# Kernel tuning notes

Measured on AMD Instinct MI355X. Metric: run time of the kernel, lower is better.

The kernel has to match this reference:

```python
import jax, jax.numpy as jnp
import numpy as np

VOCAB = 128000; D = 128; H = 4; HD = D // H; NL = 2; DOUT = 64
MAXW = 32; B = 64; L = 64; N_ITERS = 32

def _ln(x, g, b):
    m = jnp.mean(x, -1, keepdims=True)
    v = jnp.var(x, -1, keepdims=True)
    return (x - m) * jax.lax.rsqrt(v + 1e-5) * g + b

def _encoder(x, pad, p):
    # post-norm torch TransformerEncoderLayer, relu activation. x: [N,W,D], pad True=padding key
    neg = jnp.where(pad, -1e9, 0.0)[:, None, None, :]
    n = x.shape[0]
    for l in range(NL):
        qkv = x @ p["Wqkv"][l].T + p["bqkv"][l]
        q, k, v = jnp.split(qkv, 3, axis=-1)
        q = q.reshape(n, MAXW, H, HD).transpose(0, 2, 1, 3)
        k = k.reshape(n, MAXW, H, HD).transpose(0, 2, 1, 3)
        v = v.reshape(n, MAXW, H, HD).transpose(0, 2, 1, 3)
        s = jnp.einsum('nhqd,nhkd->nhqk', q, k) * (1.0 / float(np.sqrt(HD))) + neg
        o = jnp.einsum('nhqk,nhkd->nhqd', jax.nn.softmax(s, -1), v)
        o = o.transpose(0, 2, 1, 3).reshape(n, MAXW, D) @ p["Wo"][l].T + p["bo"][l]
        x = _ln(x + o, p["ln1g"][l], p["ln1b"][l])
        f = jax.nn.relu(x @ p["W1"][l].T + p["b1"][l]) @ p["W2"][l].T + p["b2"][l]
        x = _ln(x + f, p["ln2g"][l], p["ln2b"][l])
    return x

def _forward(p, token_ids, padding_mask, key):
    seq_len = jnp.sum(~padding_mask, 1).astype(jnp.int32)
    pos_idx = jnp.arange(MAXW)
    bidx = jnp.arange(B)

    def _head(x, W1h, b1h, W2h, b2h):
        return (jax.nn.relu(x @ W1h.T + b1h) @ W2h.T + b2h)[:, 0]

    def _gru(x, h):
        gi = x @ p["gru_Wih"].T + p["gru_bih"]
        gh = h @ p["gru_Whh"].T + p["gru_bhh"]
        ir, iz, inn = jnp.split(gi, 3, -1)
        hr, hz, hn = jnp.split(gh, 3, -1)
        r = jax.nn.sigmoid(ir + hr)
        z = jax.nn.sigmoid(iz + hz)
        return (1.0 - z) * jnp.tanh(inn + r * hn) + z * h

    def step(carry, k):
        win_ids, win_len, input_pos, gru_h, done = carry
        active = ~done
        pad = ~((pos_idx[None, :] < win_len[:, None]) & active[:, None])
        pad = pad.at[:, 0].set(False)  # keep softmax finite for empty windows; t1 zeroed below
        x = p["tok_emb"][win_ids] + p["pos_emb"][None, :, :]
        enc = _encoder(x, pad, p)
        last = enc[bidx, jnp.maximum(win_len - 1, 0)]
        vec = last @ p["proj_W"].T + p["proj_b"]
        vec = vec / jnp.maximum(jnp.linalg.norm(vec, axis=-1, keepdims=True), 1e-12)
        nonempty = (win_len > 0) & active
        t1 = jnp.where(nonempty[:, None], vec, 0.0)
        gru_h = jnp.where(active[:, None], _gru(t1, gru_h), gru_h)
        has_input = active & (input_pos < seq_len)
        nt = token_ids[bidx, jnp.clip(input_pos, 0, L - 1)]
        next_embs = jnp.where(has_input[:, None], p["tok_emb"][nt], 0.0)
        acc_l = _head(jnp.concatenate([next_embs, t1, gru_h], 1), p["acc_W1"], p["acc_b1"], p["acc_W2"], p["acc_b2"])
        tg = jnp.concatenate([t1, gru_h], 1)
        emt_l = _head(tg, p["emt_W1"], p["emt_b1"], p["emt_W2"], p["emt_b2"])
        evt_l = _head(tg, p["evt_W1"], p["evt_b1"], p["evt_W2"], p["evt_b2"])
        k1, k2, k3 = jax.random.split(k, 3)
        acc_s = jax.random.bernoulli(k1, jax.nn.sigmoid(acc_l))
        emt_s = jax.random.bernoulli(k2, jax.nn.sigmoid(emt_l))
        evt_s = jax.random.bernoulli(k3, jax.nn.sigmoid(evt_l))
        lp = jnp.stack([jax.nn.log_sigmoid(jnp.where(acc_s, acc_l, -acc_l)),
                        jax.nn.log_sigmoid(jnp.where(emt_s, emt_l, -emt_l)),
                        jax.nn.log_sigmoid(jnp.where(evt_s, evt_l, -evt_l))], 1)
        dec = jnp.stack([acc_s, emt_s, evt_s], 1).astype(jnp.float32)
        a = acc_s & has_input
        e = emt_s & nonempty
        v = evt_s & nonempty
        none = active & ~(a | e | v)
        a = a | (none & has_input)
        e = e | (none & ~has_input & (win_len > 0))
        a_eff = a & (win_len < MAXW)
        win_ids = jnp.where(a_eff[:, None] & (pos_idx[None, :] == win_len[:, None]), nt[:, None], win_ids)
        input_pos = input_pos + a_eff.astype(jnp.int32)
        win_len = win_len + a_eff.astype(jnp.int32)
        emit_event = e & (win_len > 0)
        v_eff = v & (win_len > 0)
        win_ids = jnp.where(v_eff[:, None], jnp.roll(win_ids, -1, axis=1), win_ids)
        win_len = win_len - v_eff.astype(jnp.int32)
        done = done | (active & (input_pos >= seq_len) & (win_len == 0))
        return (win_ids, win_len, input_pos, gru_h, done), (t1, lp, dec, emit_event)

    init = (jnp.zeros((B, MAXW), dtype=token_ids.dtype), jnp.zeros(B, jnp.int32), jnp.zeros(B, jnp.int32),
            jnp.zeros((B, D), jnp.float32), seq_len == 0)
    keys = jax.random.split(key, N_ITERS)
    _, (t1s, lps, decs, emits) = jax.lax.scan(step, init, keys)
    return t1s, lps, decs, jnp.sum(emits.astype(jnp.int32), 0)

def setup_inputs():
    key = jax.random.key(0)
    ks = jax.random.split(key, 20)
    def rn(k, shape):
        return jax.random.normal(k, shape, jnp.float32) * 0.02
    inp = {}
    inp["token_ids"] = jax.random.randint(ks[0], (B, L), 0, VOCAB)
    inp["padding_mask"] = jnp.zeros((B, L), dtype=bool)
    inp["token_instr_idx"] = jax.random.randint(ks[1], (B, L), 0, 32)
    inp["n_instructions"] = jax.random.randint(ks[2], (B,), 1, 32)
    inp["tok_emb"] = rn(ks[3], (VOCAB, D))
    inp["pos_emb"] = rn(ks[4], (MAXW, D))
    inp["Wqkv"] = rn(ks[5], (NL, 3 * D, D)); inp["bqkv"] = jnp.zeros((NL, 3 * D))
    inp["Wo"] = rn(ks[6], (NL, D, D)); inp["bo"] = jnp.zeros((NL, D))
    inp["ln1g"] = jnp.ones((NL, D)); inp["ln1b"] = jnp.zeros((NL, D))
    inp["W1"] = rn(ks[7], (NL, 4 * D, D)); inp["b1"] = jnp.zeros((NL, 4 * D))
    inp["W2"] = rn(ks[8], (NL, D, 4 * D)); inp["b2"] = jnp.zeros((NL, D))
    inp["ln2g"] = jnp.ones((NL, D)); inp["ln2b"] = jnp.zeros((NL, D))
    inp["proj_W"] = rn(ks[9], (DOUT, D)); inp["proj_b"] = jnp.zeros((DOUT,))
    inp["gru_Wih"] = rn(ks[10], (3 * D, DOUT)); inp["gru_Whh"] = rn(ks[11], (3 * D, D))
    inp["gru_bih"] = jnp.zeros((3 * D,)); inp["gru_bhh"] = jnp.zeros((3 * D,))
    inp["acc_W1"] = rn(ks[12], (D, 2 * D + DOUT)); inp["acc_b1"] = jnp.zeros((D,))
    inp["acc_W2"] = rn(ks[13], (1, D)); inp["acc_b2"] = jnp.full((1,), 2.0)
    inp["emt_W1"] = rn(ks[14], (D, D + DOUT)); inp["emt_b1"] = jnp.zeros((D,))
    inp["emt_W2"] = rn(ks[15], (1, D)); inp["emt_b2"] = jnp.full((1,), -2.0)
    inp["evt_W1"] = rn(ks[16], (D, D + DOUT)); inp["evt_b1"] = jnp.zeros((D,))
    inp["evt_W2"] = rn(ks[17], (1, D)); inp["evt_b2"] = jnp.full((1,), -2.0)
    return inp

def reference(token_ids, padding_mask, token_instr_idx, n_instructions, tok_emb, pos_emb, Wqkv, bqkv, Wo, bo, ln1g, ln1b, W1, b1, W2, b2, ln2g, ln2b, proj_W, proj_b, gru_Wih, gru_Whh, gru_bih, gru_bhh, acc_W1, acc_b1, acc_W2, acc_b2, emt_W1, emt_b1, emt_W2, emt_b2, evt_W1, evt_b1, evt_W2, evt_b2):
    p = dict(tok_emb=tok_emb, pos_emb=pos_emb, Wqkv=Wqkv, bqkv=bqkv, Wo=Wo, bo=bo, ln1g=ln1g, ln1b=ln1b,
             W1=W1, b1=b1, W2=W2, b2=b2, ln2g=ln2g, ln2b=ln2b, proj_W=proj_W, proj_b=proj_b,
             gru_Wih=gru_Wih, gru_Whh=gru_Whh, gru_bih=gru_bih, gru_bhh=gru_bhh,
             acc_W1=acc_W1, acc_b1=acc_b1, acc_W2=acc_W2, acc_b2=acc_b2,
             emt_W1=emt_W1, emt_b1=emt_b1, emt_W2=emt_W2, emt_b2=emt_b2,
             evt_W1=evt_W1, evt_b1=evt_b1, evt_W2=evt_W2, evt_b2=evt_b2)
    # token_instr_idx / n_instructions are only used for emission bookkeeping (no tensor math); unused here.
    return _forward(p, token_ids, padding_mask, jax.random.key(42))
```

## Files before the change

kernel.cpp:

```cpp
#include <hip/hip_runtime.h>
#include <hip/hip_bf16.h>


#define XS 132
#define QS 388
#define HS 516
#define PS 36
#define NW 16

struct KParams {
  const int* token_ids;
  const unsigned char* pad;
  const void *tok_emb, *pos_emb, *Wqkv, *bqkv, *Wo, *bo, *ln1g, *ln1b;
  const void *W1, *b1, *W2, *b2, *ln2g, *ln2b, *projW, *projb;
  const void *gWih, *gWhh, *gbih, *gbhh;
  const void *accW1, *accb1, *accW2, *accb2;
  const void *emtW1, *emtb1, *emtW2, *emtb2;
  const void *evtW1, *evtb1, *evtW2, *evtb2;
  float* out;
};

struct Smem {
  float xbuf[32 * XS];
  float qh[32 * HS];
  float obuf[32 * XS];
  float pbuf[4608];
  float attT[128];
  float tva[128];
  double gild[384];
  double ghld[384];
  double hsd[128];
  double t1d[64];
  double catd[320];
  double hid2d[384];
  double logitsd[3];
  int win_ids[32];
  int sI[6];
  unsigned keyts[32][2];
};

__device__ __forceinline__ float ldw(const float* p){ return *p; }
__device__ __forceinline__ float ldw(const unsigned short* p){
  return __uint_as_float(((unsigned)*p) << 16);
}
__device__ __forceinline__ float4 ld4(const float* p){ return *(const float4*)p; }
__device__ __forceinline__ float4 ld4(const unsigned short* p){
  ushort4 u = *(const ushort4*)p;
  return make_float4(__uint_as_float((unsigned)u.x << 16),
                     __uint_as_float((unsigned)u.y << 16),
                     __uint_as_float((unsigned)u.z << 16),
                     __uint_as_float((unsigned)u.w << 16));
}
template<typename WT>
__device__ __forceinline__ double ldwd(const WT* p){ return (double)ldw(p); }

__device__ __forceinline__ float temb(const void* te, int isb, long long idx){
  if (isb) return __uint_as_float(((unsigned)((const unsigned short*)te)[idx]) << 16);
  return ((const float*)te)[idx];
}

__device__ __forceinline__ void tfry(unsigned k0, unsigned k1, unsigned x0, unsigned x1,
                                     unsigned &o0, unsigned &o1){
  unsigned ks2 = k0 ^ k1 ^ 0x1BD11BDAu;
  unsigned x = x0 + k0, y = x1 + k1;
#define TFR(r) { x += y; y = (y << r) | (y >> (32 - r)); y ^= x; }
  TFR(13) TFR(15) TFR(26) TFR(6)  x += k1;  y += ks2 + 1u;
  TFR(17) TFR(29) TFR(16) TFR(24) x += ks2; y += k0 + 2u;
  TFR(13) TFR(15) TFR(26) TFR(6)  x += k0;  y += k1 + 3u;
  TFR(17) TFR(29) TFR(16) TFR(24) x += k1;  y += ks2 + 4u;
  TFR(13) TFR(15) TFR(26) TFR(6)  x += ks2; y += k0 + 5u;
#undef TFR
  o0 = x; o1 = y;
}
__device__ __forceinline__ float u01(unsigned bits){
  return __uint_as_float((bits >> 9) | 0x3f800000u) - 1.0f;
}
__device__ __forceinline__ double logsigd(double x){
  return fmin(x, 0.0) - log1p(exp(-fabs(x)));
}
__device__ __forceinline__ float wredsum(float v, int width){
  for (int m = width >> 1; m > 0; m >>= 1) v += __shfl_xor(v, m, width);
  return v;
}
__device__ __forceinline__ double wredsumd(double v, int width){
  for (int m = width >> 1; m > 0; m >>= 1) v += __shfl_xor(v, m, width);
  return v;
}
__device__ __forceinline__ float dot4f(float4 a, float4 b){
  return a.x*b.x + a.y*b.y + a.z*b.z + a.w*b.w;
}

template<int T, int K, bool RELU, typename WT>
__device__ void gemm_tok(const WT* __restrict__ Wm, const WT* __restrict__ bias,
                         int J, const float* __restrict__ xl, int xs,
                         float* __restrict__ ol, int os, int ntok,
                         int lane, int wv, int nwv)
{
  const int JBG = J >> 6;
  const int ntt = (ntok + T - 1) / T;
  for (int item = wv; item < JBG * ntt; item += nwv) {
    const int jg = item % JBG, tt = item / JBG;
    const int j0 = jg * 64 + lane;
    float acc[T];
#pragma unroll
    for (int t = 0; t < T; ++t) acc[t] = 0.f;
    const float* xr = xl + tt * T * xs;
    const WT* wr = Wm + j0 * K;
#pragma unroll 4
    for (int k = 0; k < K; k += 4) {
      float4 w = ld4(wr + k);
      float4 xv[T];
#pragma unroll
      for (int t = 0; t < T; ++t) xv[t] = *(const float4*)(xr + t * xs + k);
#pragma unroll
      for (int t = 0; t < T; ++t)
        acc[t] += w.x * xv[t].x + w.y * xv[t].y + w.z * xv[t].z + w.w * xv[t].w;
    }
    float bj = ldw(bias + j0);
#pragma unroll
    for (int t = 0; t < T; ++t) {
      int tok = tt * T + t;
      if (tok < ntok) {
        float v = acc[t] + bj;
        if (RELU) v = fmaxf(v, 0.f);
        ol[tok * os + j0] = v;
      }
    }
  }
}

template<int K, typename WT>
__device__ __forceinline__ float dotgf(const WT* __restrict__ w, const float* x){
  float acc = 0.f;
#pragma unroll 8
  for (int k = 0; k < K; k += 4) {
    float4 wv = ld4(w + k);
    acc += wv.x * x[k] + wv.y * x[k+1] + wv.z * x[k+2] + wv.w * x[k+3];
  }
  return acc;
}
template<int K, typename WT>
__device__ __forceinline__ double dotgd(const WT* __restrict__ w, const double* x){
  double acc = 0.0;
#pragma unroll 4
  for (int k = 0; k < K; k += 4) {
    float4 wv = ld4(w + k);
    acc += (double)wv.x * x[k] + (double)wv.y * x[k+1]
         + (double)wv.z * x[k+2] + (double)wv.w * x[k+3];
  }
  return acc;
}
template<int K, typename WT>
__device__ __forceinline__ double dotgdx(const WT* __restrict__ w, const float* x){
  double acc = 0.0;
#pragma unroll 4
  for (int k = 0; k < K; k += 4) {
    float4 wv = ld4(w + k);
    acc += (double)wv.x * (double)x[k] + (double)wv.y * (double)x[k+1]
         + (double)wv.z * (double)x[k+2] + (double)wv.w * (double)x[k+3];
  }
  return acc;
}

template<typename WT>
__device__ void ln_rows(float* xb, const float* ob, const WT* __restrict__ g,
                        const WT* __restrict__ bb, int W, int tid){
  if (tid >= 256) return;
  const int i = tid >> 3, sub = tid & 7;
  const int base = i * XS + sub * 16;
  float y[16];
  float s = 0.f;
#pragma unroll
  for (int u = 0; u < 16; ++u) { y[u] = xb[base + u] + ob[base + u]; s += y[u]; }
  s = wredsum(s, 8);
  const float m = s * (1.0f / 128.0f);
  float vs = 0.f;
#pragma unroll
  for (int u = 0; u < 16; ++u) { float d = y[u] - m; vs += d * d; }
  vs = wredsum(vs, 8);
  const float rstd = 1.0f / sqrtf(vs * (1.0f / 128.0f) + 1e-5f);
  if (i < W) {
#pragma unroll
    for (int u = 0; u < 16; ++u)
      xb[base + u] = (y[u] - m) * rstd * ldw(g + sub * 16 + u) + ldw(bb + sub * 16 + u);
  }
}
template<typename WT>
__device__ __forceinline__ void ln_tail(float* xrow, const float* add,
                                        const WT* __restrict__ g,
                                        const WT* __restrict__ bb, int tid){
  if (tid < 64) {
    float y0 = xrow[tid] + add[tid];
    float y1 = xrow[64 + tid] + add[64 + tid];
    float m = wredsum(y0 + y1, 64) * (1.0f / 128.0f);
    float d0 = y0 - m, d1 = y1 - m;
    float rstd = 1.0f / sqrtf(wredsum(d0 * d0 + d1 * d1, 64) * (1.0f / 128.0f) + 1e-5f);
    xrow[tid] = d0 * rstd * ldw(g + tid) + ldw(bb + tid);
    xrow[64 + tid] = d1 * rstd * ldw(g + 64 + tid) + ldw(bb + 64 + tid);
  }
}

template<typename WT>
__device__ void run_all(const KParams& P, Smem& S, int row, int tid, int isbEmb){
  const WT* pos_emb = (const WT*)P.pos_emb;
  const WT* Wqkv = (const WT*)P.Wqkv;   const WT* bqkv = (const WT*)P.bqkv;
  const WT* Wo = (const WT*)P.Wo;       const WT* bo = (const WT*)P.bo;
  const WT* ln1g = (const WT*)P.ln1g;   const WT* ln1b = (const WT*)P.ln1b;
  const WT* W1 = (const WT*)P.W1;       const WT* b1 = (const WT*)P.b1;
  const WT* W2 = (const WT*)P.W2;       const WT* b2 = (const WT*)P.b2;
  const WT* ln2g = (const WT*)P.ln2g;   const WT* ln2b = (const WT*)P.ln2b;
  const WT* projW = (const WT*)P.projW; const WT* projb = (const WT*)P.projb;
  const WT* gWih = (const WT*)P.gWih;   const WT* gWhh = (const WT*)P.gWhh;
  const WT* gbih = (const WT*)P.gbih;   const WT* gbhh = (const WT*)P.gbhh;
  const WT* accW1 = (const WT*)P.accW1; const WT* accb1 = (const WT*)P.accb1;
  const WT* accW2 = (const WT*)P.accW2; const WT* accb2 = (const WT*)P.accb2;
  const WT* emtW1 = (const WT*)P.emtW1; const WT* emtb1 = (const WT*)P.emtb1;
  const WT* emtW2 = (const WT*)P.emtW2; const WT* emtb2 = (const WT*)P.emtb2;
  const WT* evtW1 = (const WT*)P.evtW1; const WT* evtb1 = (const WT*)P.evtb1;
  const WT* evtW2 = (const WT*)P.evtW2; const WT* evtb2 = (const WT*)P.evtb2;

  const int lane = tid & 63, wid = tid >> 6;

  if (tid == 0) {
    int seq = 0;
    for (int l = 0; l < 64; ++l) seq += (P.pad[row * 64 + l] == 0);
    S.sI[0] = 0; S.sI[1] = 0; S.sI[2] = (seq == 0) ? 1 : 0; S.sI[3] = seq; S.sI[4] = 0;
  }
  if (tid < 128) S.hsd[tid] = 0.0;
  if (tid < 32) {
    S.win_ids[tid] = 0;
    unsigned a0, a1;
    tfry(0u, 42u, 0u, (unsigned)tid, a0, a1);
    S.keyts[tid][0] = a0; S.keyts[tid][1] = a1;
  }
  __syncthreads();

  for (int t = 0; t < 32; ++t) {
    const int wl = S.sI[0], ip = S.sI[1], done = S.sI[2], seq = S.sI[3];
    const int act = !done;
    const int W = wl;
    const int enc = (act && wl > 0) ? 1 : 0;
    const int jl = (W > 0) ? (W - 1) : 0;

    if (enc) {
      for (int idx = tid; idx < W * 128; idx += 1024) {
        int i = idx >> 7, d = idx & 127;
        S.xbuf[i * XS + d] = temb(P.tok_emb, isbEmb, (long long)S.win_ids[i] * 128 + d)
                             + ldw(pos_emb + i * 128 + d);
      }
      __syncthreads();
      gemm_tok<8, 128, false>(Wqkv, bqkv, 384, S.xbuf, XS, S.qh, QS, W, lane, wid, NW);
      __syncthreads();
      if (tid < 128) {
        int h = tid >> 5, i = tid & 31;
        if (i < W) {
          float4 q[8];
#pragma unroll
          for (int kk = 0; kk < 8; ++kk) q[kk] = *(const float4*)&S.qh[i * QS + h * 32 + kk * 4];
          int pb = (h * 32 + i) * PS;
          float m = -1e30f;
          for (int j = 0; j < W; ++j) {
            float s = 0.f;
#pragma unroll
            for (int kk = 0; kk < 8; ++kk)
              s += dot4f(q[kk], *(const float4*)&S.qh[j * QS + 128 + h * 32 + kk * 4]);
            s *= 0.17677669529663687f;
            S.pbuf[pb + j] = s;
            m = fmaxf(m, s);
          }
          float sum = 0.f;
          for (int j = 0; j < W; ++j) { float e = expf(S.pbuf[pb + j] - m); S.pbuf[pb + j] = e; sum += e; }
          float rs = 1.0f / sum;
          for (int j = 0; j < W; ++j) S.pbuf[pb + j] *= rs;
        }
      }
      __syncthreads();
      {
        int c = tid & 127, qsub = tid >> 7, h = c >> 5;
        for (int i = qsub; i < W; i += 8) {
          float acc = 0.f;
          for (int j = 0; j < W; ++j) acc += S.pbuf[(h * 32 + i) * PS + j] * S.qh[j * QS + 256 + c];
          S.obuf[i * XS + c] = acc;
        }
      }
      __syncthreads();
      gemm_tok<4, 128, false>(Wo, bo, 128, S.obuf, XS, S.pbuf, XS, W, lane, wid, NW);
      __syncthreads();
      ln_rows(S.xbuf, S.pbuf, ln1g, ln1b, W, tid);
      __syncthreads();
      gemm_tok<8, 128, true>(W1, b1, 512, S.xbuf, XS, S.qh, HS, W, lane, wid, NW);
      __syncthreads();
      gemm_tok<8, 512, false>(W2, b2, 128, S.qh, HS, S.obuf, XS, W, lane, wid, NW);
      __syncthreads();
      ln_rows(S.xbuf, S.obuf, ln2g, ln2b, W, tid);
      __syncthreads();
      {
        const WT* Wq = Wqkv + 384 * 128;
        const WT* bq = bqkv + 384;
        if (wid < 14) {
          gemm_tok<8, 128, false>(Wq + 128 * 128, bq + 128, 256,
                                  S.xbuf, XS, S.qh + 128, QS, W, lane, wid, 14);
        } else {
          int j = tid - 896;
          S.qh[jl * QS + j] = ldw(bq + j) + dotgf<128>(Wq + j * 128, &S.xbuf[jl * XS]);
        }
        __syncthreads();
        if (tid < 128) {
          int h = tid >> 5, j = tid & 31;
          float s = -1e30f;
          if (j < W) {
            s = 0.f;
#pragma unroll
            for (int kk = 0; kk < 8; ++kk)
              s += dot4f(*(const float4*)&S.qh[jl * QS + h * 32 + kk * 4],
                         *(const float4*)&S.qh[j * QS + 128 + h * 32 + kk * 4]);
            s *= 0.17677669529663687f;
          }
          float m = s;
          for (int mk = 16; mk; mk >>= 1) m = fmaxf(m, __shfl_xor(m, mk, 32));
          float e = (j < W) ? expf(s - m) : 0.f;
          float sum = e;
          for (int mk = 16; mk; mk >>= 1) sum += __shfl_xor(sum, mk, 32);
          if (j < W) S.pbuf[h * PS + j] = e * (1.0f / sum);
        }
        __syncthreads();
        if (tid < 128) {
          int h = tid >> 5;
          float acc = 0.f;
          for (int j = 0; j < W; ++j) acc += S.pbuf[h * PS + j] * S.qh[j * QS + 256 + tid];
          S.attT[tid] = acc;
        }
        __syncthreads();
        if (tid < 128)
          S.tva[tid] = ldw(bo + 128 + tid) + dotgf<128>(Wo + 16384 + tid * 128, S.attT);
        __syncthreads();
        ln_tail(&S.xbuf[jl * XS], S.tva, ln1g + 128, ln1b + 128, tid);
        __syncthreads();
        if (tid < 512)
          S.qh[tid] = fmaxf(ldw(b1 + 512 + tid) + dotgf<128>(W1 + (512 + tid) * 128, &S.xbuf[jl * XS]), 0.f);
        __syncthreads();
        if (tid < 128)
          S.tva[tid] = ldw(b2 + 128 + tid) + dotgf<512>(W2 + (128 + tid) * 512, S.qh);
        __syncthreads();
        ln_tail(&S.xbuf[jl * XS], S.tva, ln2g + 128, ln2b + 128, tid);
        __syncthreads();
      }
    }

    if (tid < 64) {
      double tv = 0.0;
      if (enc) {
        double v = ldwd(projb + tid) + dotgdx<128>(projW + tid * 128, &S.xbuf[jl * XS]);
        double ss = wredsumd(v * v, 64);
        tv = v / fmax(sqrt(ss), 1e-12);
      }
      S.t1d[tid] = tv;
      S.catd[128 + tid] = tv;
      P.out[(size_t)t * 4096 + row * 64 + tid] = (float)tv;
    } else if (tid >= 384 && tid < 768) {
      if (act) {
        int j = tid - 384;
        S.ghld[j] = ldwd(gbhh + j) + dotgd<128>(gWhh + j * 128, S.hsd);
      }
    } else if (tid >= 768 && tid < 896) {
      int j = tid - 768;
      int ipc = ip < 0 ? 0 : (ip > 63 ? 63 : ip);
      int nt = P.token_ids[row * 64 + ipc];
      int has_in = (act && (ip < seq)) ? 1 : 0;
      S.catd[j] = has_in ? (double)temb(P.tok_emb, isbEmb, (long long)nt * 128 + j) : 0.0;
    }
    __syncthreads();

    if (act) {
      if (tid < 384)
        S.gild[tid] = ldwd(gbih + tid) + dotgd<64>(gWih + tid * 64, S.t1d);
      __syncthreads();
    }

    if (tid < 128) {
      if (act) {
        double r = 1.0 / (1.0 + exp(-(S.gild[tid] + S.ghld[tid])));
        double z = 1.0 / (1.0 + exp(-(S.gild[128 + tid] + S.ghld[128 + tid])));
        double n = tanh(S.gild[256 + tid] + r * S.ghld[256 + tid]);
        S.hsd[tid] = (1.0 - z) * n + z * S.hsd[tid];
      }
      S.catd[192 + tid] = S.hsd[tid];
    }
    __syncthreads();

    if (tid < 128) {
      S.hid2d[tid] = fmax(ldwd(accb1 + tid) + dotgd<320>(accW1 + tid * 320, S.catd), 0.0);
    } else if (tid < 256) {
      int j = tid - 128;
      S.hid2d[128 + j] = fmax(ldwd(emtb1 + j) + dotgd<192>(emtW1 + j * 192, S.catd + 128), 0.0);
    } else if (tid < 384) {
      int j = tid - 256;
      S.hid2d[256 + j] = fmax(ldwd(evtb1 + j) + dotgd<192>(evtW1 + j * 192, S.catd + 128), 0.0);
    }
    __syncthreads();

    {
      int hw = tid >> 6;
      if (hw < 3) {
        int ln = tid & 63;
        const WT* w2 = (hw == 0) ? accW2 : ((hw == 1) ? emtW2 : evtW2);
        const WT* b2p = (hw == 0) ? accb2 : ((hw == 1) ? emtb2 : evtb2);
        double pp = S.hid2d[hw * 128 + ln] * ldwd(w2 + ln)
                  + S.hid2d[hw * 128 + 64 + ln] * ldwd(w2 + 64 + ln);
        pp = wredsumd(pp, 64);
        if (ln == 0) S.logitsd[hw] = pp + ldwd(b2p);
      }
    }
    __syncthreads();

    if (tid == 0) {
      unsigned k0 = S.keyts[t][0], k1 = S.keyts[t][1];
      unsigned sk[3][2];
      tfry(k0, k1, 0u, 0u, sk[0][0], sk[0][1]);
      tfry(k0, k1, 0u, 1u, sk[1][0], sk[1][1]);
      tfry(k0, k1, 0u, 2u, sk[2][0], sk[2][1]);
      int smp[3];
      double lg[3] = {S.logitsd[0], S.logitsd[1], S.logitsd[2]};
      for (int s = 0; s < 3; ++s) {
        unsigned r0, r1;
        tfry(sk[s][0], sk[s][1], 0u, (unsigned)row, r0, r1);
        unsigned bits = r0 ^ r1;
        double u = (double)u01(bits);
        double p = 1.0 / (1.0 + exp(-lg[s]));
        smp[s] = (u < p) ? 1 : 0;
        P.out[131072 + (size_t)t * 192 + row * 3 + s] = (float)logsigd(smp[s] ? lg[s] : -lg[s]);
        P.out[137216 + (size_t)t * 192 + row * 3 + s] = smp[s] ? 1.0f : 0.0f;
      }
      int wl2 = wl, ip2 = ip, dn = done;
      int nonempty = (wl2 > 0) && act;
      int has_in = act && (ip2 < seq);
      int a = smp[0] && has_in;
      int e = smp[1] && nonempty;
      int v = smp[2] && nonempty;
      int none = act && !(a || e || v);
      a = a || (none && has_in);
      e = e || (none && !has_in && (wl2 > 0));
      int aeff = a && (wl2 < 32);
      int ipc = ip2 < 0 ? 0 : (ip2 > 63 ? 63 : ip2);
      int nt = P.token_ids[row * 64 + ipc];
      if (aeff) { S.win_ids[wl2] = nt; ip2 += 1; wl2 += 1; }
      int emit = e && (wl2 > 0);
      S.sI[4] += emit;
      int veff = v && (wl2 > 0);
      if (veff) {
        int w0 = S.win_ids[0];
#pragma unroll
        for (int i2 = 0; i2 < 31; ++i2) S.win_ids[i2] = S.win_ids[i2 + 1];
        S.win_ids[31] = w0;
        wl2 -= 1;
      }
      if (act && (ip2 >= seq) && (wl2 == 0)) dn = 1;
      S.sI[0] = wl2; S.sI[1] = ip2; S.sI[2] = dn;
    }
    __syncthreads();
  }
  if (tid == 0) P.out[143360 + row] = (float)S.sI[4];
}

__global__ __launch_bounds__(1024) void src_main_kernel(KParams P){
  __shared__ __align__(16) Smem S;
  const int row = blockIdx.x;
  const int tid = threadIdx.x;
  const bool isb = (((const unsigned short*)P.ln1g)[0] == (unsigned short)0x3F80);
  if (isb) run_all<unsigned short>(P, S, row, tid, 1);
  else     run_all<float>(P, S, row, tid, 0);
}

extern "C" void kernel_launch(void* const* d_in, const int* in_sizes, int n_in,
                              void* d_out, int out_size, void* d_ws, size_t ws_size,
                              hipStream_t stream) {
  KParams P;
  P.token_ids = (const int*)d_in[0];
  P.pad = (const unsigned char*)d_in[1];
  P.tok_emb = d_in[4];  P.pos_emb = d_in[5];
  P.Wqkv = d_in[6];     P.bqkv = d_in[7];
  P.Wo = d_in[8];       P.bo = d_in[9];
  P.ln1g = d_in[10];    P.ln1b = d_in[11];
  P.W1 = d_in[12];      P.b1 = d_in[13];
  P.W2 = d_in[14];      P.b2 = d_in[15];
  P.ln2g = d_in[16];    P.ln2b = d_in[17];
  P.projW = d_in[18];   P.projb = d_in[19];
  P.gWih = d_in[20];    P.gWhh = d_in[21];
  P.gbih = d_in[22];    P.gbhh = d_in[23];
  P.accW1 = d_in[24];   P.accb1 = d_in[25];
  P.accW2 = d_in[26];   P.accb2 = d_in[27];
  P.emtW1 = d_in[28];   P.emtb1 = d_in[29];
  P.emtW2 = d_in[30];   P.emtb2 = d_in[31];
  P.evtW1 = d_in[32];   P.evtb1 = d_in[33];
  P.evtW2 = d_in[34];   P.evtb2 = d_in[35];
  P.out = (float*)d_out;
  hipLaunchKernelGGL(src_main_kernel, dim3(64), dim3(1024), 0, stream, P);
}
```

Measured before the change: 4.656 ms.

## Split dot products across more threads, double GEMM output per lane, vectorise loads

Several unrelated changes land together. The token GEMM now computes two output columns per lane so each activation load from shared memory is reused twice. The embedding gather and layer norm use float4 loads. The attention probability buffer is transposed so the PV product reads float4 and applies softmax normalisation at the end. Serial per-thread dot products for the tail encoder, GRU and heads are split over 2-4 lanes and combined with shuffle reductions, and the three Bernoulli samples are drawn in parallel lanes. Together these aim to cut latency in the long single-block sequential loop, at the cost of more register pressure in the GEMM and a changed floating-point summation order.

```diff
diff --git a/kernel.cpp b/kernel.cpp
--- a/kernel.cpp
+++ b/kernel.cpp
@@ -7,6 +7,7 @@
 #define HS 516
 #define PS 36
 #define NW 16
+#define PT 132
 
 struct KParams {
   const int* token_ids;
@@ -91,39 +92,42 @@
 }
 
 template<int T, int K, bool RELU, typename WT>
-__device__ void gemm_tok(const WT* __restrict__ Wm, const WT* __restrict__ bias,
-                         int J, const float* __restrict__ xl, int xs,
-                         float* __restrict__ ol, int os, int ntok,
-                         int lane, int wv, int nwv)
+__device__ void gemm_tok2(const WT* __restrict__ Wm, const WT* __restrict__ bias,
+                          int J, const float* __restrict__ xl, int xs,
+                          float* __restrict__ ol, int os, int ntok,
+                          int lane, int wv, int nwv)
 {
-  const int JBG = J >> 6;
+  const int JP = J >> 7;
   const int ntt = (ntok + T - 1) / T;
-  for (int item = wv; item < JBG * ntt; item += nwv) {
-    const int jg = item % JBG, tt = item / JBG;
-    const int j0 = jg * 64 + lane;
-    float acc[T];
-#pragma unroll
-    for (int t = 0; t < T; ++t) acc[t] = 0.f;
+  for (int item = wv; item < JP * ntt; item += nwv) {
+    const int jp = item % JP, tt = item / JP;
+    const int j0 = jp * 128 + lane;
+    float acc0[T], acc1[T];
+#pragma unroll
+    for (int t = 0; t < T; ++t) { acc0[t] = 0.f; acc1[t] = 0.f; }
     const float* xr = xl + tt * T * xs;
-    const WT* wr = Wm + j0 * K;
-#pragma unroll 4
+    const WT* wr0 = Wm + (size_t)j0 * K;
+    const WT* wr1 = wr0 + (size_t)64 * K;
+#pragma unroll 2
     for (int k = 0; k < K; k += 4) {
-      float4 w = ld4(wr + k);
-      float4 xv[T];
-#pragma unroll
-      for (int t = 0; t < T; ++t) xv[t] = *(const float4*)(xr + t * xs + k);
-#pragma unroll
-      for (int t = 0; t < T; ++t)
-        acc[t] += w.x * xv[t].x + w.y * xv[t].y + w.z * xv[t].z + w.w * xv[t].w;
-    }
-    float bj = ldw(bias + j0);
+      float4 w0 = ld4(wr0 + k);
+      float4 w1 = ld4(wr1 + k);
+#pragma unroll
+      for (int t = 0; t < T; ++t) {
+        float4 xv = *(const float4*)(xr + t * xs + k);
+        acc0[t] += w0.x * xv.x + w0.y * xv.y + w0.z * xv.z + w0.w * xv.w;
+        acc1[t] += w1.x * xv.x + w1.y * xv.y + w1.z * xv.z + w1.w * xv.w;
+      }
+    }
+    float b0 = ldw(bias + j0), b1v = ldw(bias + j0 + 64);
 #pragma unroll
     for (int t = 0; t < T; ++t) {
       int tok = tt * T + t;
       if (tok < ntok) {
-        float v = acc[t] + bj;
-        if (RELU) v = fmaxf(v, 0.f);
-        ol[tok * os + j0] = v;
+        float v0 = acc0[t] + b0, v1 = acc1[t] + b1v;
+        if (RELU) { v0 = fmaxf(v0, 0.f); v1 = fmaxf(v1, 0.f); }
+        ol[tok * os + j0] = v0;
+        ol[tok * os + j0 + 64] = v1;
       }
     }
   }
@@ -142,7 +146,7 @@
 template<int K, typename WT>
 __device__ __forceinline__ double dotgd(const WT* __restrict__ w, const double* x){
   double acc = 0.0;
-#pragma unroll 4
+#pragma unroll 8
   for (int k = 0; k < K; k += 4) {
     float4 wv = ld4(w + k);
     acc += (double)wv.x * x[k] + (double)wv.y * x[k+1]
@@ -153,7 +157,7 @@
 template<int K, typename WT>
 __device__ __forceinline__ double dotgdx(const WT* __restrict__ w, const float* x){
   double acc = 0.0;
-#pragma unroll 4
+#pragma unroll 8
   for (int k = 0; k < K; k += 4) {
     float4 wv = ld4(w + k);
     acc += (double)wv.x * (double)x[k] + (double)wv.y * (double)x[k+1]
@@ -171,7 +175,12 @@
   float y[16];
   float s = 0.f;
 #pragma unroll
-  for (int u = 0; u < 16; ++u) { y[u] = xb[base + u] + ob[base + u]; s += y[u]; }
+  for (int u = 0; u < 16; u += 4) {
+    float4 xv = *(const float4*)(xb + base + u);
+    float4 ov = *(const float4*)(ob + base + u);
+    y[u] = xv.x + ov.x; y[u+1] = xv.y + ov.y; y[u+2] = xv.z + ov.z; y[u+3] = xv.w + ov.w;
+    s += y[u] + y[u+1] + y[u+2] + y[u+3];
+  }
   s = wredsum(s, 8);
   const float m = s * (1.0f / 128.0f);
   float vs = 0.f;
@@ -181,8 +190,16 @@
   const float rstd = 1.0f / sqrtf(vs * (1.0f / 128.0f) + 1e-5f);
   if (i < W) {
 #pragma unroll
-    for (int u = 0; u < 16; ++u)
-      xb[base + u] = (y[u] - m) * rstd * ldw(g + sub * 16 + u) + ldw(bb + sub * 16 + u);
+    for (int u = 0; u < 16; u += 4) {
+      float4 gg = ld4(g + sub * 16 + u);
+      float4 bv = ld4(bb + sub * 16 + u);
+      float4 r;
+      r.x = (y[u]   - m) * rstd * gg.x + bv.x;
+      r.y = (y[u+1] - m) * rstd * gg.y + bv.y;
+      r.z = (y[u+2] - m) * rstd * gg.z + bv.z;
+      r.w = (y[u+3] - m) * rstd * gg.w + bv.w;
+      *(float4*)(xb + base + u) = r;
+    }
   }
 }
 template<typename WT>
@@ -202,6 +219,7 @@
 
 template<typename WT>
 __device__ void run_all(const KParams& P, Smem& S, int row, int tid, int isbEmb){
+  const WT* tok_embw = (const WT*)P.tok_emb;
   const WT* pos_emb = (const WT*)P.pos_emb;
   const WT* Wqkv = (const WT*)P.Wqkv;   const WT* bqkv = (const WT*)P.bqkv;
   const WT* Wo = (const WT*)P.Wo;       const WT* bo = (const WT*)P.bo;
@@ -243,13 +261,20 @@
     const int jl = (W > 0) ? (W - 1) : 0;
 
     if (enc) {
-      for (int idx = tid; idx < W * 128; idx += 1024) {
-        int i = idx >> 7, d = idx & 127;
-        S.xbuf[i * XS + d] = temb(P.tok_emb, isbEmb, (long long)S.win_ids[i] * 128 + d)
-                             + ldw(pos_emb + i * 128 + d);
-      }
-      __syncthreads();
-      gemm_tok<8, 128, false>(Wqkv, bqkv, 384, S.xbuf, XS, S.qh, QS, W, lane, wid, NW);
+      for (int idx = tid; idx < W * 16; idx += 1024) {
+        int i = idx >> 4, d0 = (idx & 15) << 3;
+        const WT* te = tok_embw + (long long)S.win_ids[i] * 128 + d0;
+        const WT* pe = pos_emb + (size_t)i * 128 + d0;
+        float4 t0 = ld4(te), t1 = ld4(te + 4), p0 = ld4(pe), p1 = ld4(pe + 4);
+        float* dst = &S.xbuf[i * XS + d0];
+        float4 r0, r1;
+        r0.x = t0.x + p0.x; r0.y = t0.y + p0.y; r0.z = t0.z + p0.z; r0.w = t0.w + p0.w;
+        r1.x = t1.x + p1.x; r1.y = t1.y + p1.y; r1.z = t1.z + p1.z; r1.w = t1.w + p1.w;
+        *(float4*)dst = r0;
+        *(float4*)(dst + 4) = r1;
+      }
+      __syncthreads();
+      gemm_tok2<8, 128, false>(Wqkv, bqkv, 384, S.xbuf, XS, S.qh, QS, W, lane, wid, NW);
       __syncthreads();
       if (tid < 128) {
         int h = tid >> 5, i = tid & 31;
@@ -257,7 +282,6 @@
           float4 q[8];
 #pragma unroll
           for (int kk = 0; kk < 8; ++kk) q[kk] = *(const float4*)&S.qh[i * QS + h * 32 + kk * 4];
-          int pb = (h * 32 + i) * PS;
           float m = -1e30f;
           for (int j = 0; j < W; ++j) {
             float s = 0.f;
@@ -265,32 +289,42 @@
             for (int kk = 0; kk < 8; ++kk)
               s += dot4f(q[kk], *(const float4*)&S.qh[j * QS + 128 + h * 32 + kk * 4]);
             s *= 0.17677669529663687f;
-            S.pbuf[pb + j] = s;
+            S.pbuf[j * PT + tid] = s;
             m = fmaxf(m, s);
           }
           float sum = 0.f;
-          for (int j = 0; j < W; ++j) { float e = expf(S.pbuf[pb + j] - m); S.pbuf[pb + j] = e; sum += e; }
-          float rs = 1.0f / sum;
-          for (int j = 0; j < W; ++j) S.pbuf[pb + j] *= rs;
+          for (int j = 0; j < W; ++j) {
+            float e = expf(S.pbuf[j * PT + tid] - m);
+            S.pbuf[j * PT + tid] = e;
+            sum += e;
+          }
+          S.pbuf[32 * PT + tid] = 1.0f / sum;
         }
       }
       __syncthreads();
       {
-        int c = tid & 127, qsub = tid >> 7, h = c >> 5;
-        for (int i = qsub; i < W; i += 8) {
-          float acc = 0.f;
-          for (int j = 0; j < W; ++j) acc += S.pbuf[(h * 32 + i) * PS + j] * S.qh[j * QS + 256 + c];
-          S.obuf[i * XS + c] = acc;
-        }
-      }
-      __syncthreads();
-      gemm_tok<4, 128, false>(Wo, bo, 128, S.obuf, XS, S.pbuf, XS, W, lane, wid, NW);
+        int c = tid & 127, g = tid >> 7;
+        int h = c >> 5, ib = g * 4;
+        float a0 = 0.f, a1 = 0.f, a2 = 0.f, a3 = 0.f;
+        for (int j = 0; j < W; ++j) {
+          float4 p = *(const float4*)&S.pbuf[j * PT + h * 32 + ib];
+          float v = S.qh[j * QS + 256 + c];
+          a0 += p.x * v; a1 += p.y * v; a2 += p.z * v; a3 += p.w * v;
+        }
+        float4 rs = *(const float4*)&S.pbuf[32 * PT + h * 32 + ib];
+        if (ib + 0 < W) S.obuf[(ib + 0) * XS + c] = a0 * rs.x;
+        if (ib + 1 < W) S.obuf[(ib + 1) * XS + c] = a1 * rs.y;
+        if (ib + 2 < W) S.obuf[(ib + 2) * XS + c] = a2 * rs.z;
+        if (ib + 3 < W) S.obuf[(ib + 3) * XS + c] = a3 * rs.w;
+      }
+      __syncthreads();
+      gemm_tok2<4, 128, false>(Wo, bo, 128, S.obuf, XS, S.pbuf, XS, W, lane, wid, NW);
       __syncthreads();
       ln_rows(S.xbuf, S.pbuf, ln1g, ln1b, W, tid);
       __syncthreads();
-      gemm_tok<8, 128, true>(W1, b1, 512, S.xbuf, XS, S.qh, HS, W, lane, wid, NW);
-      __syncthreads();
-      gemm_tok<8, 512, false>(W2, b2, 128, S.qh, HS, S.obuf, XS, W, lane, wid, NW);
+      gemm_tok2<8, 128, true>(W1, b1, 512, S.xbuf, XS, S.qh, HS, W, lane, wid, NW);
+      __syncthreads();
+      gemm_tok2<8, 512, false>(W2, b2, 128, S.qh, HS, S.obuf, XS, W, lane, wid, NW);
       __syncthreads();
       ln_rows(S.xbuf, S.obuf, ln2g, ln2b, W, tid);
       __syncthreads();
@@ -298,8 +332,8 @@
         const WT* Wq = Wqkv + 384 * 128;
         const WT* bq = bqkv + 384;
         if (wid < 14) {
-          gemm_tok<8, 128, false>(Wq + 128 * 128, bq + 128, 256,
-                                  S.xbuf, XS, S.qh + 128, QS, W, lane, wid, 14);
+          gemm_tok2<8, 128, false>(Wq + 128 * 128, bq + 128, 256,
+                                   S.xbuf, XS, S.qh + 128, QS, W, lane, wid, 14);
         } else {
           int j = tid - 896;
           S.qh[jl * QS + j] = ldw(bq + j) + dotgf<128>(Wq + j * 128, &S.xbuf[jl * XS]);
@@ -331,16 +365,30 @@
           S.attT[tid] = acc;
         }
         __syncthreads();
-        if (tid < 128)
-          S.tva[tid] = ldw(bo + 128 + tid) + dotgf<128>(Wo + 16384 + tid * 128, S.attT);
+        if (tid < 512) {
+          int j = tid >> 2, q = tid & 3;
+          float v = dotgf<32>(Wo + 16384 + (size_t)j * 128 + q * 32, S.attT + q * 32);
+          v += __shfl_xor(v, 1, 64);
+          v += __shfl_xor(v, 2, 64);
+          if (q == 0) S.tva[j] = ldw(bo + 128 + j) + v;
+        }
         __syncthreads();
         ln_tail(&S.xbuf[jl * XS], S.tva, ln1g + 128, ln1b + 128, tid);
         __syncthreads();
-        if (tid < 512)
-          S.qh[tid] = fmaxf(ldw(b1 + 512 + tid) + dotgf<128>(W1 + (512 + tid) * 128, &S.xbuf[jl * XS]), 0.f);
-        __syncthreads();
-        if (tid < 128)
-          S.tva[tid] = ldw(b2 + 128 + tid) + dotgf<512>(W2 + (128 + tid) * 512, S.qh);
+        {
+          int j = tid >> 1, h = tid & 1;
+          float v = dotgf<64>(W1 + (size_t)(512 + j) * 128 + h * 64, &S.xbuf[jl * XS] + h * 64);
+          v += __shfl_xor(v, 1, 64);
+          if (h == 0) S.qh[j] = fmaxf(ldw(b1 + 512 + j) + v, 0.f);
+        }
+        __syncthreads();
+        if (tid < 512) {
+          int j = tid >> 2, q = tid & 3;
+          float v = dotgf<128>(W2 + (size_t)(128 + j) * 512 + q * 128, S.qh + q * 128);
+          v += __shfl_xor(v, 1, 64);
+          v += __shfl_xor(v, 2, 64);
+          if (q == 0) S.tva[j] = ldw(b2 + 128 + j) + v;
+        }
         __syncthreads();
         ln_tail(&S.xbuf[jl * XS], S.tva, ln2g + 128, ln2b + 128, tid);
         __syncthreads();
@@ -357,13 +405,16 @@
       S.t1d[tid] = tv;
       S.catd[128 + tid] = tv;
       P.out[(size_t)t * 4096 + row * 64 + tid] = (float)tv;
-    } else if (tid >= 384 && tid < 768) {
+    } else if (tid >= 128 && tid < 896) {
       if (act) {
-        int j = tid - 384;
-        S.ghld[j] = ldwd(gbhh + j) + dotgd<128>(gWhh + j * 128, S.hsd);
-      }
-    } else if (tid >= 768 && tid < 896) {
-      int j = tid - 768;
+        int jj = tid - 128;
+        int j = jj >> 1, h = jj & 1;
+        double v = dotgd<64>(gWhh + (size_t)j * 128 + h * 64, S.hsd + h * 64);
+        v += __shfl_xor(v, 1, 64);
+        if (h == 0) S.ghld[j] = ldwd(gbhh + j) + v;
+      }
+    } else if (tid >= 896) {
+      int j = tid - 896;
       int ipc = ip < 0 ? 0 : (ip > 63 ? 63 : ip);
       int nt = P.token_ids[row * 64 + ipc];
       int has_in = (act && (ip < seq)) ? 1 : 0;
@@ -372,8 +423,12 @@
     __syncthreads();
 
     if (act) {
-      if (tid < 384)
-        S.gild[tid] = ldwd(gbih + tid) + dotgd<64>(gWih + tid * 64, S.t1d);
+      if (tid < 768) {
+        int j = tid >> 1, h = tid & 1;
+        double v = dotgd<32>(gWih + (size_t)j * 64 + h * 32, S.t1d + h * 32);
+        v += __shfl_xor(v, 1, 64);
+        if (h == 0) S.gild[j] = ldwd(gbih + j) + v;
+      }
       __syncthreads();
     }
 
@@ -388,14 +443,24 @@
     }
     __syncthreads();
 
-    if (tid < 128) {
-      S.hid2d[tid] = fmax(ldwd(accb1 + tid) + dotgd<320>(accW1 + tid * 320, S.catd), 0.0);
-    } else if (tid < 256) {
-      int j = tid - 128;
-      S.hid2d[128 + j] = fmax(ldwd(emtb1 + j) + dotgd<192>(emtW1 + j * 192, S.catd + 128), 0.0);
-    } else if (tid < 384) {
-      int j = tid - 256;
-      S.hid2d[256 + j] = fmax(ldwd(evtb1 + j) + dotgd<192>(evtW1 + j * 192, S.catd + 128), 0.0);
+    if (tid < 768) {
+      int jo = tid >> 1, h = tid & 1;
+      double v;
+      if (jo < 128) {
+        v = dotgd<160>(accW1 + (size_t)jo * 320 + h * 160, S.catd + h * 160);
+      } else if (jo < 256) {
+        int j = jo - 128;
+        v = dotgd<96>(emtW1 + (size_t)j * 192 + h * 96, S.catd + 128 + h * 96);
+      } else {
+        int j = jo - 256;
+        v = dotgd<96>(evtW1 + (size_t)j * 192 + h * 96, S.catd + 128 + h * 96);
+      }
+      v += __shfl_xor(v, 1, 64);
+      if (h == 0) {
+        double b = (jo < 128) ? ldwd(accb1 + jo)
+                 : (jo < 256 ? ldwd(emtb1 + jo - 128) : ldwd(evtb1 + jo - 256));
+        S.hid2d[jo] = fmax(b + v, 0.0);
+      }
     }
     __syncthreads();
 
@@ -413,49 +478,50 @@
     }
     __syncthreads();
 
-    if (tid == 0) {
+    if (tid < 64) {
       unsigned k0 = S.keyts[t][0], k1 = S.keyts[t][1];
-      unsigned sk[3][2];
-      tfry(k0, k1, 0u, 0u, sk[0][0], sk[0][1]);
-      tfry(k0, k1, 0u, 1u, sk[1][0], sk[1][1]);
-      tfry(k0, k1, 0u, 2u, sk[2][0], sk[2][1]);
-      int smp[3];
-      double lg[3] = {S.logitsd[0], S.logitsd[1], S.logitsd[2]};
-      for (int s = 0; s < 3; ++s) {
-        unsigned r0, r1;
-        tfry(sk[s][0], sk[s][1], 0u, (unsigned)row, r0, r1);
-        unsigned bits = r0 ^ r1;
-        double u = (double)u01(bits);
-        double p = 1.0 / (1.0 + exp(-lg[s]));
-        smp[s] = (u < p) ? 1 : 0;
-        P.out[131072 + (size_t)t * 192 + row * 3 + s] = (float)logsigd(smp[s] ? lg[s] : -lg[s]);
-        P.out[137216 + (size_t)t * 192 + row * 3 + s] = smp[s] ? 1.0f : 0.0f;
-      }
-      int wl2 = wl, ip2 = ip, dn = done;
-      int nonempty = (wl2 > 0) && act;
-      int has_in = act && (ip2 < seq);
-      int a = smp[0] && has_in;
-      int e = smp[1] && nonempty;
-      int v = smp[2] && nonempty;
-      int none = act && !(a || e || v);
-      a = a || (none && has_in);
-      e = e || (none && !has_in && (wl2 > 0));
-      int aeff = a && (wl2 < 32);
-      int ipc = ip2 < 0 ? 0 : (ip2 > 63 ? 63 : ip2);
-      int nt = P.token_ids[row * 64 + ipc];
-      if (aeff) { S.win_ids[wl2] = nt; ip2 += 1; wl2 += 1; }
-      int emit = e && (wl2 > 0);
-      S.sI[4] += emit;
-      int veff = v && (wl2 > 0);
-      if (veff) {
-        int w0 = S.win_ids[0];
-#pragma unroll
-        for (int i2 = 0; i2 < 31; ++i2) S.win_ids[i2] = S.win_ids[i2 + 1];
-        S.win_ids[31] = w0;
-        wl2 -= 1;
-      }
-      if (act && (ip2 >= seq) && (wl2 == 0)) dn = 1;
-      S.sI[0] = wl2; S.sI[1] = ip2; S.sI[2] = dn;
+      int smp_l = 0;
+      if (tid < 3) {
+        double lgv = S.logitsd[tid];
+        unsigned sk0, sk1, r0, r1;
+        tfry(k0, k1, 0u, (unsigned)tid, sk0, sk1);
+        tfry(sk0, sk1, 0u, (unsigned)row, r0, r1);
+        double u = (double)u01(r0 ^ r1);
+        double p = 1.0 / (1.0 + exp(-lgv));
+        smp_l = (u < p) ? 1 : 0;
+        P.out[131072 + (size_t)t * 192 + row * 3 + tid] = (float)logsigd(smp_l ? lgv : -lgv);
+        P.out[137216 + (size_t)t * 192 + row * 3 + tid] = smp_l ? 1.0f : 0.0f;
+      }
+      int sa = __shfl(smp_l, 0, 64);
+      int se = __shfl(smp_l, 1, 64);
+      int sv = __shfl(smp_l, 2, 64);
+      if (tid == 0) {
+        int wl2 = wl, ip2 = ip, dn = done;
+        int nonempty = (wl2 > 0) && act;
+        int has_in = act && (ip2 < seq);
+        int a = sa && has_in;
+        int e = se && nonempty;
+        int v = sv && nonempty;
+        int none = act && !(a || e || v);
+        a = a || (none && has_in);
+        e = e || (none && !has_in && (wl2 > 0));
+        int aeff = a && (wl2 < 32);
+        int ipc = ip2 < 0 ? 0 : (ip2 > 63 ? 63 : ip2);
+        int nt = P.token_ids[row * 64 + ipc];
+        if (aeff) { S.win_ids[wl2] = nt; ip2 += 1; wl2 += 1; }
+        int emit = e && (wl2 > 0);
+        S.sI[4] += emit;
+        int veff = v && (wl2 > 0);
+        if (veff) {
+          int w0 = S.win_ids[0];
+#pragma unroll
+          for (int i2 = 0; i2 < 31; ++i2) S.win_ids[i2] = S.win_ids[i2 + 1];
+          S.win_ids[31] = w0;
+          wl2 -= 1;
+        }
+        if (act && (ip2 >= seq) && (wl2 == 0)) dn = 1;
+        S.sI[0] = wl2; S.sI[1] = ip2; S.sI[2] = dn;
+      }
     }
     __syncthreads();
   }
```

After: 5.211 ms. +11.9%, slower.
